# Optimization experiments

Hardware: AMD Instinct MI355X
Metric: run time of the kernel (lower is better)

The kernel has to match this reference:

```python
import jax, jax.numpy as jnp
import numpy as np

N, E, F_IN, NCLS, H = 50000, 800000, 128, 10, 64


def setup_inputs() -> dict:
    key = jax.random.key(0)
    ks = jax.random.split(key, 24)
    p = lambda k, shp: (jax.random.normal(k, shp, dtype=jnp.float32) * 0.1)
    inp = {
        'x': jax.random.normal(ks[0], (N, F_IN), dtype=jnp.float32),
        'edge_index': jax.random.randint(ks[1], (2, E), 0, N, dtype=jnp.int64),
        'gcn1_W': p(ks[2], (F_IN, 128)), 'gcn1_b': p(ks[3], (128,)),
        'gcn2_W': p(ks[4], (128, 64)),  'gcn2_b': p(ks[5], (64,)),
        'gcn3_W': p(ks[6], (64, 32)),   'gcn3_b': p(ks[7], (32,)),
        'gat_W': p(ks[8], (32, 32)), 'gat_a_src': p(ks[9], (32,)),
        'gat_a_dst': p(ks[10], (32,)), 'gat_b': p(ks[11], (32,)),
        'lstm_Wih_f': p(ks[12], (4 * H, 32)), 'lstm_bih_f': p(ks[13], (4 * H,)), 'lstm_bhh_f': p(ks[14], (4 * H,)),
        'lstm_Wih_b': p(ks[15], (4 * H, 32)), 'lstm_bih_b': p(ks[16], (4 * H,)), 'lstm_bhh_b': p(ks[17], (4 * H,)),
        'bn_gamma': jnp.ones((2 * H,), jnp.float32), 'bn_beta': jnp.zeros((2 * H,), jnp.float32),
        'fc_W': p(ks[18], (NCLS, 2 * H)), 'fc_b': p(ks[19], (NCLS,)),
    }
    return inp


def _forward(x, edge_index, gcn1_W, gcn1_b, gcn2_W, gcn2_b, gcn3_W, gcn3_b,
             gat_W, gat_a_src, gat_a_dst, gat_b,
             lstm_Wih_f, lstm_bih_f, lstm_bhh_f, lstm_Wih_b, lstm_bih_b, lstm_bhh_b,
             bn_gamma, bn_beta, fc_W, fc_b):
    n = x.shape[0]
    loop = jnp.arange(n)
    row = jnp.concatenate([edge_index[0], loop])  # source nodes (+ self loops)
    col = jnp.concatenate([edge_index[1], loop])  # target nodes
    deg = jax.ops.segment_sum(jnp.ones_like(col, dtype=x.dtype), col, num_segments=n)
    dis = jax.lax.rsqrt(jnp.maximum(deg, 1e-12))  # deg >= 1 due to self loops
    norm = dis[row] * dis[col]

    def gcn(h, W, b):
        h = h @ W
        return jax.ops.segment_sum(h[row] * norm[:, None], col, num_segments=n) + b

    h = jax.nn.relu(gcn(x, gcn1_W, gcn1_b))
    h = jax.nn.relu(gcn(h, gcn2_W, gcn2_b))
    h = gcn(h, gcn3_W, gcn3_b)

    # GAT (1 head), self loops already in row/col, softmax over incoming edges per target
    g = h @ gat_W
    e = jax.nn.leaky_relu((g @ gat_a_src)[row] + (g @ gat_a_dst)[col], negative_slope=0.2)
    m = jax.ops.segment_max(e, col, num_segments=n)
    ee = jnp.exp(e - m[col])
    att = ee / jax.ops.segment_sum(ee, col, num_segments=n)[col]
    h = jax.ops.segment_sum(g[row] * att[:, None], col, num_segments=n) + gat_b
    h = jax.nn.relu(h)

    # bidirectional LSTM with seq_len=1, h0=c0=0 -> single cell step per direction
    def lstm_dir(xx, Wih, bih, bhh):
        gt = xx @ Wih.T + bih + bhh
        i, f, c, o = jnp.split(gt, 4, axis=-1)  # torch gate order i,f,g,o
        return jax.nn.sigmoid(o) * jnp.tanh(jax.nn.sigmoid(i) * jnp.tanh(c))

    r = jnp.concatenate([lstm_dir(h, lstm_Wih_f, lstm_bih_f, lstm_bhh_f),
                         lstm_dir(h, lstm_Wih_b, lstm_bih_b, lstm_bhh_b)], axis=-1)
    # eval mode: dropout = identity; BatchNorm1d with running_mean=0, running_var=1
    r = r * (bn_gamma / jnp.sqrt(jnp.float32(1.0 + 1e-5))) + bn_beta
    return r @ fc_W.T + fc_b


def reference(x, edge_index, gcn1_W, gcn1_b, gcn2_W, gcn2_b, gcn3_W, gcn3_b,
              gat_W, gat_a_src, gat_a_dst, gat_b,
              lstm_Wih_f, lstm_bih_f, lstm_bhh_f, lstm_Wih_b, lstm_bih_b, lstm_bhh_b,
              bn_gamma, bn_beta, fc_W, fc_b):
    return _forward(x, edge_index, gcn1_W, gcn1_b, gcn2_W, gcn2_b, gcn3_W, gcn3_b,
                    gat_W, gat_a_src, gat_a_dst, gat_b,
                    lstm_Wih_f, lstm_bih_f, lstm_bhh_f, lstm_Wih_b, lstm_bih_b, lstm_bhh_b,
                    bn_gamma, bn_beta, fc_W, fc_b)
```

## Files before the change

### kernel.cpp

```cpp
#include <hip/hip_runtime.h>
#include <hip/hip_bf16.h>
#include <math.h>

typedef __hip_bfloat16 bf16;

#define NN 50000
#define EE 800000
#define EPB 4096
#define NBK 196
#define BCAP 6144

__device__ __forceinline__ float b2f(bf16 v) { return __bfloat162float(v); }
__device__ __forceinline__ float rcp_(float x) { return __builtin_amdgcn_rcpf(x); }
__device__ __forceinline__ float sigmoidf_(float x) { return rcp_(1.0f + __expf(-x)); }
__device__ __forceinline__ float tanhf_(float x) {
    float xx = fminf(fmaxf(x, -15.0f), 15.0f);
    float e = __expf(2.0f * xx);
    return (e - 1.0f) * rcp_(e + 1.0f);
}
__device__ __forceinline__ float leakyf_(float x) { return x > 0.0f ? x : 0.2f * x; }
__device__ __forceinline__ unsigned short f2bf(float f) {
    unsigned u = __float_as_uint(f);
    unsigned r = (u + 0x7FFFu + ((u >> 16) & 1u)) >> 16;
    return (unsigned short)r;
}
__device__ __forceinline__ unsigned pack2(float a, float b) {
    return (unsigned)f2bf(a) | ((unsigned)f2bf(b) << 16);
}
__device__ __forceinline__ float lo_(unsigned u) { return __uint_as_float(u << 16); }
__device__ __forceinline__ float hi_(unsigned u) { return __uint_as_float(u & 0xFFFF0000u); }

#define OFF_W1 0
#define OFF_B1 16384
#define OFF_W2 16512
#define OFF_B2 24704
#define OFF_W3 24768
#define OFF_B3 26816
#define OFF_GATW 26848
#define OFF_GAS 27872
#define OFF_GAD 27904
#define OFF_GAB 27936
#define OFF_WIHF 27968
#define OFF_BIHF 36160
#define OFF_BHHF 36416
#define OFF_WIHB 36672
#define OFF_BIHB 44864
#define OFF_BHHB 45120
#define OFF_GAMMA 45376
#define OFF_BETA 45504
#define OFF_FCW 45632
#define OFF_FCB 46912
#define WTOTAL 46922

struct WSrc { const void* p[20]; };

__global__ void k_detect(const unsigned short* __restrict__ xraw,
                         const unsigned int* __restrict__ eraw, int* __restrict__ flags) {
    __shared__ int f32f, i64f;
    int t = threadIdx.x;
    if (t == 0) { f32f = 0; i64f = 1; }
    __syncthreads();
    for (int i = t; i < 4096; i += 256) {
        unsigned short u = xraw[i];
        int ex = (u >> 7) & 0xFF;
        if (ex >= 0xC0) atomicOr(&f32f, 1);
        if (eraw[2 * i + 1] != 0u) atomicAnd(&i64f, 0);
    }
    __syncthreads();
    if (t == 0) { flags[0] = f32f; flags[1] = i64f; }
}

__global__ void k_cvt_w(WSrc srcs, float* __restrict__ dst, const int* __restrict__ flags,
                        int total) {
    constexpr int WOFF[21] = {OFF_W1,   OFF_B1,   OFF_W2,   OFF_B2,   OFF_W3,   OFF_B3,
                              OFF_GATW, OFF_GAS,  OFF_GAD,  OFF_GAB,  OFF_WIHF, OFF_BIHF,
                              OFF_BHHF, OFF_WIHB, OFF_BIHB, OFF_BHHB, OFF_GAMMA, OFF_BETA,
                              OFF_FCW,  OFF_FCB,  WTOTAL};
    int i = blockIdx.x * 256 + threadIdx.x;
    if (i >= total) return;
    int tn = 0;
#pragma unroll
    for (int j = 1; j < 20; ++j)
        if (i >= WOFF[j]) tn = j;
    int local = i - WOFF[tn];
    if (flags[0]) dst[i] = ((const float*)srcs.p[tn])[local];
    else dst[i] = b2f(((const bf16*)srcs.p[tn])[local]);
}

__global__ __launch_bounds__(256) void k_hist(const void* __restrict__ eraw,
                                              unsigned* __restrict__ gh,
                                              const int* __restrict__ flags) {
    __shared__ int h[256];
    int t = threadIdx.x, b = blockIdx.x;
    h[t] = 0;
    __syncthreads();
    int e0 = b * EPB;
    bool i64 = flags[1] != 0;
    for (int i = t; i < EPB; i += 256) {
        int e = e0 + i;
        if (e < EE) {
            int d = i64 ? (int)((const long long*)eraw)[EE + e] : ((const int*)eraw)[EE + e];
            d = min(max(d, 0), NN - 1);
            atomicAdd(&h[d >> 8], 1);
        }
    }
    __syncthreads();
    gh[b * 256 + t] = (unsigned)h[t];
}

__global__ __launch_bounds__(256) void k_bscan(const unsigned* __restrict__ gh,
                                               unsigned* __restrict__ gh2,
                                               int* __restrict__ bb, int* __restrict__ rptr) {
    __shared__ int s[256];
    int t = threadIdx.x;
    unsigned run = 0;
    for (int blk = 0; blk < NBK; ++blk) {
        unsigned v = gh[blk * 256 + t];
        gh2[blk * 256 + t] = run;
        run += v;
    }
    s[t] = (int)run;
    __syncthreads();
    for (int o = 1; o < 256; o <<= 1) {
        int x = (t >= o) ? s[t - o] : 0;
        __syncthreads();
        s[t] += x;
        __syncthreads();
    }
    bb[t] = s[t] - (int)run;
    if (t == 0) rptr[NN] = EE;
}

__global__ __launch_bounds__(256) void k_scatter(const void* __restrict__ eraw,
                                                 const unsigned* __restrict__ gh2,
                                                 const int* __restrict__ bb,
                                                 int2* __restrict__ ebkt,
                                                 const int* __restrict__ flags) {
    __shared__ unsigned cur[256];
    int t = threadIdx.x, b = blockIdx.x;
    cur[t] = gh2[b * 256 + t] + (unsigned)bb[t];
    __syncthreads();
    int e0 = b * EPB;
    bool i64 = flags[1] != 0;
    for (int i = t; i < EPB; i += 256) {
        int e = e0 + i;
        if (e < EE) {
            int sn, d;
            if (i64) {
                sn = (int)((const long long*)eraw)[e];
                d = (int)((const long long*)eraw)[EE + e];
            } else {
                sn = ((const int*)eraw)[e];
                d = ((const int*)eraw)[EE + e];
            }
            sn = min(max(sn, 0), NN - 1);
            d = min(max(d, 0), NN - 1);
            unsigned pos = atomicAdd(&cur[d >> 8], 1u);
            if (pos < (unsigned)EE) ebkt[pos] = make_int2(sn, d);
        }
    }
}

__global__ __launch_bounds__(256) void k_bucket_csr(const int2* __restrict__ ebkt,
                                                    const int* __restrict__ bb,
                                                    int* __restrict__ rptr,
                                                    float* __restrict__ dis,
                                                    int* __restrict__ csr_src) {
    __shared__ int hist[256];
    __shared__ int excl[256];
    __shared__ int cur[256];
    __shared__ int sorted[BCAP];
    int t = threadIdx.x, b = blockIdx.x;
    int s0 = bb[b], s1 = bb[b + 1];
    int len = min(s1 - s0, BCAP);
    hist[t] = 0;
    __syncthreads();
    for (int i = t; i < len; i += 256) atomicAdd(&hist[ebkt[s0 + i].y & 255], 1);
    __syncthreads();
    int v = hist[t];
    excl[t] = v;
    __syncthreads();
    for (int o = 1; o < 256; o <<= 1) {
        int x = (t >= o) ? excl[t - o] : 0;
        __syncthreads();
        excl[t] += x;
        __syncthreads();
    }
    int loc = excl[t] - v;
    int node = b * 256 + t;
    if (node < NN) {
        rptr[node] = s0 + loc;
        dis[node] = rsqrtf((float)(v + 1));
    }
    cur[t] = loc;
    __syncthreads();
    for (int i = t; i < len; i += 256) {
        int2 p = ebkt[s0 + i];
        int pos = atomicAdd(&cur[p.y & 255], 1);
        if (pos < BCAP) sorted[pos] = p.x;
    }
    __syncthreads();
    for (int i = t; i < len; i += 256) csr_src[s0 + i] = sorted[i];
}

template <int KIN, int KOUT, int MODE, bool SCALE>
__global__ __launch_bounds__(256) void k_tile_mm(const void* __restrict__ A,
                                                 const float* __restrict__ W,
                                                 unsigned* __restrict__ C, int n,
                                                 const int* __restrict__ flags, int want,
                                                 const float* __restrict__ dis) {
    if (want >= 0 && flags[0] != want) return;
    constexpr int BK = 32;
    constexpr int AST = BK + 4;
    constexpr int CPT = KOUT / 16;
    __shared__ float As[64 * AST];
    __shared__ float Ws[BK * KOUT];
    int t = threadIdx.x;
    int jc = t & 15;
    int ng = t >> 4;
    int base = blockIdx.x * 64;
    float acc[4][CPT];
#pragma unroll
    for (int i = 0; i < 4; ++i)
#pragma unroll
        for (int c = 0; c < CPT; ++c) acc[i][c] = 0.f;
    int snode = t >> 2;
    int gnode = min(base + snode, n - 1);
    int koff = (t & 3) * 8;
    for (int k0 = 0; k0 < KIN; k0 += BK) {
        {
            const float4* src = (const float4*)(W + k0 * KOUT);
            float4* dst = (float4*)Ws;
#pragma unroll
            for (int p = 0; p < BK * KOUT / 1024; ++p) dst[t + p * 256] = src[t + p * 256];
        }
        if (MODE == 0) {
            const unsigned* xr = (const unsigned*)A + (size_t)gnode * (KIN / 2) + (k0 + koff) / 2;
            unsigned u0 = xr[0], u1 = xr[1], u2 = xr[2], u3 = xr[3];
            float* d = As + snode * AST + koff;
            d[0] = lo_(u0); d[1] = hi_(u0);
            d[2] = lo_(u1); d[3] = hi_(u1);
            d[4] = lo_(u2); d[5] = hi_(u2);
            d[6] = lo_(u3); d[7] = hi_(u3);
        } else {
            const float4* ar = (const float4*)((const float*)A + (size_t)gnode * KIN + k0 + koff);
            float4 v0 = ar[0], v1 = ar[1];
            float4* d = (float4*)(As + snode * AST + koff);
            d[0] = v0;
            d[1] = v1;
        }
        __syncthreads();
#pragma unroll 8
        for (int k = 0; k < BK; ++k) {
            float w[CPT];
            const float* wr = Ws + k * KOUT + jc * CPT;
            if constexpr (CPT >= 4) {
#pragma unroll
                for (int c = 0; c < CPT; c += 4) {
                    float4 wv = *(const float4*)(wr + c);
                    w[c] = wv.x; w[c + 1] = wv.y; w[c + 2] = wv.z; w[c + 3] = wv.w;
                }
            } else {
                float2 wv = *(const float2*)wr;
                w[0] = wv.x; w[1] = wv.y;
            }
            float a0 = As[(ng * 4 + 0) * AST + k];
            float a1 = As[(ng * 4 + 1) * AST + k];
            float a2 = As[(ng * 4 + 2) * AST + k];
            float a3 = As[(ng * 4 + 3) * AST + k];
#pragma unroll
            for (int c = 0; c < CPT; ++c) {
                acc[0][c] += a0 * w[c];
                acc[1][c] += a1 * w[c];
                acc[2][c] += a2 * w[c];
                acc[3][c] += a3 * w[c];
            }
        }
        __syncthreads();
    }
#pragma unroll
    for (int i = 0; i < 4; ++i) {
        int node = base + ng * 4 + i;
        if (node < n) {
            float sc = SCALE ? dis[node] : 1.0f;
            unsigned* cr = C + (size_t)node * (KOUT / 2) + jc * (CPT / 2);
#pragma unroll
            for (int c = 0; c < CPT; c += 2)
                cr[c / 2] = pack2(acc[i][c] * sc, acc[i][c + 1] * sc);
        }
    }
}

template <bool RELU>
__global__ void k_agg128(const unsigned* __restrict__ t, const int* __restrict__ rptr,
                         const int* __restrict__ csr_src, const float* __restrict__ dis,
                         const float* __restrict__ bias, float* __restrict__ out, int n) {
    int wave = (blockIdx.x * blockDim.x + threadIdx.x) >> 6;
    int lane = threadIdx.x & 63;
    if (wave >= n) return;
    int dst = wave;
    float dd = dis[dst];
    float ax, ay;
    {
        unsigned u = t[(size_t)dst * 64 + lane];
        ax = lo_(u);
        ay = hi_(u);
    }
    int s = __builtin_amdgcn_readfirstlane(max(0, min(rptr[dst], EE)));
    int e = __builtin_amdgcn_readfirstlane(max(s, min(rptr[dst + 1], EE)));
    int j = s;
    for (; j + 8 <= e; j += 8) {
        int i0 = csr_src[j], i1 = csr_src[j + 1], i2 = csr_src[j + 2], i3 = csr_src[j + 3];
        int i4 = csr_src[j + 4], i5 = csr_src[j + 5], i6 = csr_src[j + 6], i7 = csr_src[j + 7];
        unsigned u0 = t[(size_t)i0 * 64 + lane], u1 = t[(size_t)i1 * 64 + lane];
        unsigned u2 = t[(size_t)i2 * 64 + lane], u3 = t[(size_t)i3 * 64 + lane];
        unsigned u4 = t[(size_t)i4 * 64 + lane], u5 = t[(size_t)i5 * 64 + lane];
        unsigned u6 = t[(size_t)i6 * 64 + lane], u7 = t[(size_t)i7 * 64 + lane];
        ax += (lo_(u0) + lo_(u1)) + (lo_(u2) + lo_(u3)) + (lo_(u4) + lo_(u5)) + (lo_(u6) + lo_(u7));
        ay += (hi_(u0) + hi_(u1)) + (hi_(u2) + hi_(u3)) + (hi_(u4) + hi_(u5)) + (hi_(u6) + hi_(u7));
    }
    for (; j + 4 <= e; j += 4) {
        int i0 = csr_src[j], i1 = csr_src[j + 1], i2 = csr_src[j + 2], i3 = csr_src[j + 3];
        unsigned u0 = t[(size_t)i0 * 64 + lane], u1 = t[(size_t)i1 * 64 + lane];
        unsigned u2 = t[(size_t)i2 * 64 + lane], u3 = t[(size_t)i3 * 64 + lane];
        ax += (lo_(u0) + lo_(u1)) + (lo_(u2) + lo_(u3));
        ay += (hi_(u0) + hi_(u1)) + (hi_(u2) + hi_(u3));
    }
    for (; j < e; ++j) {
        unsigned u0 = t[(size_t)csr_src[j] * 64 + lane];
        ax += lo_(u0);
        ay += hi_(u0);
    }
    float2 bv = *(const float2*)(bias + 2 * lane);
    float vx = ax * dd + bv.x;
    float vy = ay * dd + bv.y;
    if (RELU) { vx = fmaxf(vx, 0.f); vy = fmaxf(vy, 0.f); }
    *(float2*)(out + (size_t)dst * 128 + 2 * lane) = make_float2(vx, vy);
}

template <bool RELU>
__global__ void k_agg64(const unsigned* __restrict__ t, const int* __restrict__ rptr,
                        const int* __restrict__ csr_src, const float* __restrict__ dis,
                        const float* __restrict__ bias, float* __restrict__ out, int n) {
    int wave = (blockIdx.x * blockDim.x + threadIdx.x) >> 6;
    int lane = threadIdx.x & 63;
    if (wave >= n) return;
    int dst = wave;
    int half = lane >> 5, l32 = lane & 31;
    float dd = dis[dst];
    float ax = 0.f, ay = 0.f;
    if (!half) {
        unsigned u = t[(size_t)dst * 32 + l32];
        ax = lo_(u);
        ay = hi_(u);
    }
    int s = max(0, min(rptr[dst], EE));
    int e = max(s, min(rptr[dst + 1], EE));
    int cnt = e - s;
    int pairs = cnt >> 1;
    int p = 0;
    for (; p + 4 <= pairs; p += 4) {
        int jb = s + 2 * p + half;
        int i0 = csr_src[jb], i1 = csr_src[jb + 2], i2 = csr_src[jb + 4], i3 = csr_src[jb + 6];
        unsigned u0 = t[(size_t)i0 * 32 + l32], u1 = t[(size_t)i1 * 32 + l32];
        unsigned u2 = t[(size_t)i2 * 32 + l32], u3 = t[(size_t)i3 * 32 + l32];
        ax += (lo_(u0) + lo_(u1)) + (lo_(u2) + lo_(u3));
        ay += (hi_(u0) + hi_(u1)) + (hi_(u2) + hi_(u3));
    }
    for (; p < pairs; ++p) {
        int i0 = csr_src[s + 2 * p + half];
        unsigned u0 = t[(size_t)i0 * 32 + l32];
        ax += lo_(u0);
        ay += hi_(u0);
    }
    if ((cnt & 1) && !half) {
        unsigned u0 = t[(size_t)csr_src[e - 1] * 32 + l32];
        ax += lo_(u0);
        ay += hi_(u0);
    }
    ax += __shfl_down(ax, 32);
    ay += __shfl_down(ay, 32);
    if (!half) {
        float2 bv = *(const float2*)(bias + 2 * l32);
        float vx = ax * dd + bv.x;
        float vy = ay * dd + bv.y;
        if (RELU) { vx = fmaxf(vx, 0.f); vy = fmaxf(vy, 0.f); }
        *(float2*)(out + (size_t)dst * 64 + 2 * l32) = make_float2(vx, vy);
    }
}

template <bool RELU>
__global__ void k_agg32(const unsigned* __restrict__ t, const int* __restrict__ rptr,
                        const int* __restrict__ csr_src, const float* __restrict__ dis,
                        const float* __restrict__ bias, float* __restrict__ out, int n) {
    int wave = (blockIdx.x * blockDim.x + threadIdx.x) >> 6;
    int lane = threadIdx.x & 63;
    if (wave >= n) return;
    int dst = wave;
    int q = lane >> 4, l16 = lane & 15;
    float dd = dis[dst];
    float ax = 0.f, ay = 0.f;
    if (q == 0) {
        unsigned u = t[(size_t)dst * 16 + l16];
        ax = lo_(u);
        ay = hi_(u);
    }
    int s = max(0, min(rptr[dst], EE));
    int e = max(s, min(rptr[dst + 1], EE));
    int cnt = e - s;
    int quads = cnt >> 2;
    int p = 0;
    for (; p + 4 <= quads; p += 4) {
        int jb = s + 4 * p + q;
        int i0 = csr_src[jb], i1 = csr_src[jb + 4], i2 = csr_src[jb + 8], i3 = csr_src[jb + 12];
        unsigned u0 = t[(size_t)i0 * 16 + l16], u1 = t[(size_t)i1 * 16 + l16];
        unsigned u2 = t[(size_t)i2 * 16 + l16], u3 = t[(size_t)i3 * 16 + l16];
        ax += (lo_(u0) + lo_(u1)) + (lo_(u2) + lo_(u3));
        ay += (hi_(u0) + hi_(u1)) + (hi_(u2) + hi_(u3));
    }
    for (; p < quads; ++p) {
        int i0 = csr_src[s + 4 * p + q];
        unsigned u0 = t[(size_t)i0 * 16 + l16];
        ax += lo_(u0);
        ay += hi_(u0);
    }
    int rem = cnt - 4 * quads;
    if (q < rem) {
        unsigned u0 = t[(size_t)csr_src[s + 4 * quads + q] * 16 + l16];
        ax += lo_(u0);
        ay += hi_(u0);
    }
    ax += __shfl_down(ax, 32);
    ay += __shfl_down(ay, 32);
    ax += __shfl_down(ax, 16);
    ay += __shfl_down(ay, 16);
    if (q == 0) {
        float2 bv = *(const float2*)(bias + 2 * l16);
        float vx = ax * dd + bv.x;
        float vy = ay * dd + bv.y;
        if (RELU) { vx = fmaxf(vx, 0.f); vy = fmaxf(vy, 0.f); }
        *(float2*)(out + (size_t)dst * 32 + 2 * l16) = make_float2(vx, vy);
    }
}

__global__ void k_gat_vec(const unsigned* __restrict__ g, const float* __restrict__ a_src,
                          const float* __restrict__ a_dst, float* __restrict__ asrc,
                          float* __restrict__ adst, int n) {
    int i = blockIdx.x * 256 + threadIdx.x;
    if (i >= n) return;
    float s = 0.0f, d = 0.0f;
    const unsigned* gr = g + (size_t)i * 16;
#pragma unroll
    for (int k = 0; k < 16; ++k) {
        unsigned u = gr[k];
        float v0 = lo_(u), v1 = hi_(u);
        s += v0 * a_src[2 * k] + v1 * a_src[2 * k + 1];
        d += v0 * a_dst[2 * k] + v1 * a_dst[2 * k + 1];
    }
    asrc[i] = s;
    adst[i] = d;
}

__global__ void k_gat_agg(const unsigned* __restrict__ g, const int* __restrict__ rptr,
                          const int* __restrict__ csr_src, const float* __restrict__ asrc,
                          const float* __restrict__ adst, const float* __restrict__ gat_b,
                          float* __restrict__ out, int n) {
    int wave = (blockIdx.x * blockDim.x + threadIdx.x) >> 6;
    int lane = threadIdx.x & 63;
    if (wave >= n) return;
    int dst = wave;
    int q = lane >> 4, l16 = lane & 15;
    float ad = adst[dst];
    int s = max(0, min(rptr[dst], EE));
    int e = max(s, min(rptr[dst + 1], EE));
    float ax = 0.f, ay = 0.f, denom = 0.f;
    if (q == 0) {
        float w0 = __expf(fminf(leakyf_(asrc[dst] + ad), 80.f));
        unsigned u = g[(size_t)dst * 16 + l16];
        ax = lo_(u) * w0;
        ay = hi_(u) * w0;
        denom = w0;
    }
    int cnt = e - s;
    int quads = cnt >> 2;
    int p = 0;
    for (; p + 4 <= quads; p += 4) {
        int jb = s + 4 * p + q;
        int i0 = csr_src[jb], i1 = csr_src[jb + 4], i2 = csr_src[jb + 8], i3 = csr_src[jb + 12];
        float a0 = asrc[i0], a1 = asrc[i1], a2 = asrc[i2], a3 = asrc[i3];
        unsigned u0 = g[(size_t)i0 * 16 + l16], u1 = g[(size_t)i1 * 16 + l16];
        unsigned u2 = g[(size_t)i2 * 16 + l16], u3 = g[(size_t)i3 * 16 + l16];
        float w0 = __expf(fminf(leakyf_(a0 + ad), 80.f));
        float w1 = __expf(fminf(leakyf_(a1 + ad), 80.f));
        float w2 = __expf(fminf(leakyf_(a2 + ad), 80.f));
        float w3 = __expf(fminf(leakyf_(a3 + ad), 80.f));
        denom += (w0 + w1) + (w2 + w3);
        ax += lo_(u0) * w0 + lo_(u1) * w1 + lo_(u2) * w2 + lo_(u3) * w3;
        ay += hi_(u0) * w0 + hi_(u1) * w1 + hi_(u2) * w2 + hi_(u3) * w3;
    }
    for (; p < quads; ++p) {
        int i0 = csr_src[s + 4 * p + q];
        float wgt = __expf(fminf(leakyf_(asrc[i0] + ad), 80.f));
        unsigned u0 = g[(size_t)i0 * 16 + l16];
        denom += wgt;
        ax += lo_(u0) * wgt;
        ay += hi_(u0) * wgt;
    }
    int rem = cnt - 4 * quads;
    if (q < rem) {
        int i0 = csr_src[s + 4 * quads + q];
        float wgt = __expf(fminf(leakyf_(asrc[i0] + ad), 80.f));
        unsigned u0 = g[(size_t)i0 * 16 + l16];
        denom += wgt;
        ax += lo_(u0) * wgt;
        ay += hi_(u0) * wgt;
    }
    ax += __shfl_down(ax, 32);
    ay += __shfl_down(ay, 32);
    denom += __shfl_down(denom, 32);
    ax += __shfl_down(ax, 16);
    ay += __shfl_down(ay, 16);
    denom += __shfl_down(denom, 16);
    if (q == 0) {
        float r = rcp_(denom);
        float vx = fmaxf(ax * r + gat_b[2 * l16], 0.f);
        float vy = fmaxf(ay * r + gat_b[2 * l16 + 1], 0.f);
        *(float2*)(out + (size_t)dst * 32 + 2 * l16) = make_float2(vx, vy);
    }
}

__global__ __launch_bounds__(128) void k_lstm_fc(const float* __restrict__ h,
                                                 const float* __restrict__ wp,
                                                 void* __restrict__ out,
                                                 const int* __restrict__ flags, int n) {
    __shared__ float hs[32 * 32];
    __shared__ float rs[32 * 129];
    __shared__ float fcw[1280];
    __shared__ float ps[32 * 40];
    int t = threadIdx.x;
    int base = blockIdx.x * 32;
    for (int idx = t; idx < 256; idx += 128) {
        int nd = idx >> 3, k4 = idx & 7;
        int node = min(base + nd, n - 1);
        ((float4*)hs)[idx] = ((const float4*)(h + (size_t)node * 32))[k4];
    }
    for (int i = t; i < 1280; i += 128) fcw[i] = wp[OFF_FCW + i];
    __syncthreads();
    {
        int dir = t >> 6, j = t & 63;
        const float* W = wp + (dir ? OFF_WIHB : OFF_WIHF);
        const float* bi = wp + (dir ? OFF_BIHB : OFF_BIHF);
        const float* bh = wp + (dir ? OFF_BHHB : OFF_BHHF);
        float wi[32], wc[32], wo[32];
#pragma unroll
        for (int k = 0; k < 32; ++k) {
            wi[k] = W[j * 32 + k];
            wc[k] = W[(128 + j) * 32 + k];
            wo[k] = W[(192 + j) * 32 + k];
        }
        float bI = bi[j] + bh[j];
        float bC = bi[128 + j] + bh[128 + j];
        float bO = bi[192 + j] + bh[192 + j];
        float gsc = wp[OFF_GAMMA + t] * rsqrtf(1.0f + 1e-5f);
        float gbe = wp[OFF_BETA + t];
#pragma unroll 2
        for (int nn = 0; nn < 32; ++nn) {
            const float* hv = hs + nn * 32;
            float ai = bI, ac = bC, ao = bO;
#pragma unroll
            for (int k = 0; k < 32; ++k) {
                float hk = hv[k];
                ai += hk * wi[k];
                ac += hk * wc[k];
                ao += hk * wo[k];
            }
            float v = sigmoidf_(ao) * tanhf_(sigmoidf_(ai) * tanhf_(ac));
            rs[nn * 129 + t] = v * gsc + gbe;
        }
    }
    __syncthreads();
    {
        int nd = t & 31, q = t >> 5;
        float p10[10];
#pragma unroll
        for (int c = 0; c < 10; ++c) p10[c] = 0.f;
#pragma unroll
        for (int k = 0; k < 32; ++k) {
            float rv = rs[nd * 129 + q * 32 + k];
#pragma unroll
            for (int c = 0; c < 10; ++c) p10[c] += rv * fcw[c * 128 + q * 32 + k];
        }
#pragma unroll
        for (int c = 0; c < 10; ++c) ps[nd * 40 + q * 10 + c] = p10[c];
    }
    __syncthreads();
    for (int idx = t; idx < 320; idx += 128) {
        int nd = idx / 10, c = idx % 10;
        int node = base + nd;
        if (node < n) {
            float v = wp[OFF_FCB + c] + ps[nd * 40 + c] + ps[nd * 40 + 10 + c] +
                      ps[nd * 40 + 20 + c] + ps[nd * 40 + 30 + c];
            if (flags[0]) ((float*)out)[(size_t)node * 10 + c] = v;
            else ((bf16*)out)[(size_t)node * 10 + c] = __float2bfloat16(v);
        }
    }
}

extern "C" void kernel_launch(void* const* d_in, const int* in_sizes, int n_in,
                              void* d_out, int out_size, void* d_ws, size_t ws_size,
                              hipStream_t stream) {
    const int N = NN;

    char* w = (char*)d_ws;
    auto alloc = [&](size_t bytes) {
        void* p = (void*)w;
        w += (bytes + 255) & ~(size_t)255;
        return p;
    };
    int* flags = (int*)alloc(256);
    float* wpool = (float*)alloc((size_t)WTOTAL * 4);
    float* dis = (float*)alloc((size_t)N * 4);
    int* rptr = (int*)alloc((size_t)(N + 1) * 4);
    int* csr_src = (int*)alloc((size_t)EE * 4);
    unsigned* gh = (unsigned*)alloc((size_t)NBK * 256 * 4);
    unsigned* gh2 = (unsigned*)alloc((size_t)NBK * 256 * 4);
    int* bb = (int*)alloc(1024);
    int2* ebkt = (int2*)alloc((size_t)EE * 8);
    float* asrc = (float*)alloc((size_t)N * 4);
    float* adst = (float*)alloc((size_t)N * 4);
    unsigned* bufT = (unsigned*)alloc((size_t)N * 64 * 4);
    float* bufH = (float*)alloc((size_t)N * 128 * 4);

    WSrc ws_srcs;
    for (int i = 0; i < 20; ++i) ws_srcs.p[i] = d_in[2 + i];

    const int NB = (N + 255) / 256;
    const int AGG = (N + 3) / 4;
    const int TMB = (N + 63) / 64;
    const int LFB = (N + 31) / 32;
    const int WB = (WTOTAL + 255) / 256;

    k_detect<<<1, 256, 0, stream>>>((const unsigned short*)d_in[0],
                                    (const unsigned int*)d_in[1], flags);
    k_cvt_w<<<WB, 256, 0, stream>>>(ws_srcs, wpool, flags, WTOTAL);
    k_hist<<<NBK, 256, 0, stream>>>(d_in[1], gh, flags);
    k_bscan<<<1, 256, 0, stream>>>(gh, gh2, bb, rptr);
    k_scatter<<<NBK, 256, 0, stream>>>(d_in[1], gh2, bb, ebkt, flags);
    k_bucket_csr<<<NBK, 256, 0, stream>>>(ebkt, bb, rptr, dis, csr_src);

    k_tile_mm<128, 128, 0, true><<<TMB, 256, 0, stream>>>(d_in[0], wpool + OFF_W1, bufT, N, flags, 0, dis);
    k_tile_mm<128, 128, 1, true><<<TMB, 256, 0, stream>>>(d_in[0], wpool + OFF_W1, bufT, N, flags, 1, dis);
    k_agg128<true><<<AGG, 256, 0, stream>>>(bufT, rptr, csr_src, dis, wpool + OFF_B1, bufH, N);
    k_tile_mm<128, 64, 1, true><<<TMB, 256, 0, stream>>>(bufH, wpool + OFF_W2, bufT, N, flags, -1, dis);
    k_agg64<true><<<AGG, 256, 0, stream>>>(bufT, rptr, csr_src, dis, wpool + OFF_B2, bufH, N);
    k_tile_mm<64, 32, 1, true><<<TMB, 256, 0, stream>>>(bufH, wpool + OFF_W3, bufT, N, flags, -1, dis);
    k_agg32<false><<<AGG, 256, 0, stream>>>(bufT, rptr, csr_src, dis, wpool + OFF_B3, bufH, N);
    k_tile_mm<32, 32, 1, false><<<TMB, 256, 0, stream>>>(bufH, wpool + OFF_GATW, bufT, N, flags, -1, dis);
    k_gat_vec<<<NB, 256, 0, stream>>>(bufT, wpool + OFF_GAS, wpool + OFF_GAD, asrc, adst, N);
    k_gat_agg<<<AGG, 256, 0, stream>>>(bufT, rptr, csr_src, asrc, adst, wpool + OFF_GAB, bufH, N);
    k_lstm_fc<<<LFB, 128, 0, stream>>>(bufH, wpool, d_out, flags, N);
}
```

Before: 380.1 us.

## Split LSTM+FC into register-tiled gate GEMM kernel and separate FC kernel

Replaces the fused LSTM/FC kernel with a preprocessing step that packs the i/c/o gate weights into an interleaved layout. A register-tiled gate kernel then stages the weights in shared memory and computes 4 nodes x 24 gate columns per thread. This targets the low-reuse per-thread dot products in the old 128-thread kernel, where each thread held 96 weights in registers. The cost is a 128-float-per-node intermediate written to global memory and read back by a new FC kernel, plus the extra workspace buffers.

```diff
diff --git a/kernel.cpp b/kernel.cpp
--- a/kernel.cpp
+++ b/kernel.cpp
@@ -87,6 +87,29 @@
     else dst[i] = b2f(((const bf16*)srcs.p[tn])[local]);
 }
 
+__global__ void k_prep(const float* __restrict__ wp, float* __restrict__ wg,
+                       float* __restrict__ bg) {
+    int i = blockIdx.x * 256 + threadIdx.x;
+    if (i < 384) {
+        int jc = i / 24, rr = i % 24, r = rr / 3, g = rr % 3;
+        int f = jc * 8 + r;
+        int dir = f >> 6, j = f & 63;
+        int grow = (g == 0) ? j : ((g == 1) ? 128 + j : 192 + j);
+        int obi = dir ? OFF_BIHB : OFF_BIHF;
+        int obh = dir ? OFF_BHHB : OFF_BHHF;
+        bg[i] = wp[obi + grow] + wp[obh + grow];
+    }
+    if (i < 12288) {
+        int k = i / 384, col = i % 384;
+        int jc = col / 24, rr = col % 24, r = rr / 3, g = rr % 3;
+        int f = jc * 8 + r;
+        int dir = f >> 6, j = f & 63;
+        int grow = (g == 0) ? j : ((g == 1) ? 128 + j : 192 + j);
+        int ow = dir ? OFF_WIHB : OFF_WIHF;
+        wg[i] = wp[ow + grow * 32 + k];
+    }
+}
+
 __global__ __launch_bounds__(256) void k_hist(const void* __restrict__ eraw,
                                               unsigned* __restrict__ gh,
                                               const int* __restrict__ flags) {
@@ -287,6 +310,127 @@
 #pragma unroll
             for (int c = 0; c < CPT; c += 2)
                 cr[c / 2] = pack2(acc[i][c] * sc, acc[i][c + 1] * sc);
+        }
+    }
+}
+
+__global__ __launch_bounds__(256, 2) void k_gates(const float* __restrict__ h,
+                                                  const float* __restrict__ wg,
+                                                  const float* __restrict__ bg,
+                                                  const float* __restrict__ wp,
+                                                  float* __restrict__ r, int n) {
+    __shared__ float Ws[32 * 384];
+    __shared__ float As[64 * 36];
+    int t = threadIdx.x;
+    int jc = t & 15, ng = t >> 4;
+    int base = blockIdx.x * 64;
+    {
+        const float4* src = (const float4*)wg;
+        float4* dst = (float4*)Ws;
+#pragma unroll
+        for (int p = 0; p < 12; ++p) dst[t + p * 256] = src[t + p * 256];
+    }
+    {
+        int snode = t >> 2;
+        int gnode = min(base + snode, n - 1);
+        int koff = (t & 3) * 8;
+        const float4* ar = (const float4*)(h + (size_t)gnode * 32 + koff);
+        float4 v0 = ar[0], v1 = ar[1];
+        float4* d = (float4*)(As + snode * 36 + koff);
+        d[0] = v0;
+        d[1] = v1;
+    }
+    float acc[4][24];
+#pragma unroll
+    for (int c = 0; c < 24; ++c) {
+        float b = bg[jc * 24 + c];
+        acc[0][c] = b; acc[1][c] = b; acc[2][c] = b; acc[3][c] = b;
+    }
+    float gsc[8], gbe[8];
+    const float bnscale = rsqrtf(1.0f + 1e-5f);
+#pragma unroll
+    for (int rc = 0; rc < 8; ++rc) {
+        gsc[rc] = wp[OFF_GAMMA + jc * 8 + rc] * bnscale;
+        gbe[rc] = wp[OFF_BETA + jc * 8 + rc];
+    }
+    __syncthreads();
+#pragma unroll 4
+    for (int k = 0; k < 32; ++k) {
+        float w[24];
+        const float* wr = Ws + k * 384 + jc * 24;
+#pragma unroll
+        for (int c = 0; c < 24; c += 4) {
+            float4 wv = *(const float4*)(wr + c);
+            w[c] = wv.x; w[c + 1] = wv.y; w[c + 2] = wv.z; w[c + 3] = wv.w;
+        }
+        float a0 = As[(ng * 4 + 0) * 36 + k];
+        float a1 = As[(ng * 4 + 1) * 36 + k];
+        float a2 = As[(ng * 4 + 2) * 36 + k];
+        float a3 = As[(ng * 4 + 3) * 36 + k];
+#pragma unroll
+        for (int c = 0; c < 24; ++c) {
+            acc[0][c] += a0 * w[c];
+            acc[1][c] += a1 * w[c];
+            acc[2][c] += a2 * w[c];
+            acc[3][c] += a3 * w[c];
+        }
+    }
+#pragma unroll
+    for (int i = 0; i < 4; ++i) {
+        int node = base + ng * 4 + i;
+        if (node >= n) continue;
+        float vals[8];
+#pragma unroll
+        for (int rc = 0; rc < 8; ++rc) {
+            float gi = acc[i][3 * rc], gc = acc[i][3 * rc + 1], go = acc[i][3 * rc + 2];
+            float v = sigmoidf_(go) * tanhf_(sigmoidf_(gi) * tanhf_(gc));
+            vals[rc] = v * gsc[rc] + gbe[rc];
+        }
+        float* rr = r + (size_t)node * 128 + jc * 8;
+        *(float4*)rr = make_float4(vals[0], vals[1], vals[2], vals[3]);
+        *(float4*)(rr + 4) = make_float4(vals[4], vals[5], vals[6], vals[7]);
+    }
+}
+
+__global__ __launch_bounds__(256) void k_fc(const float* __restrict__ r,
+                                            const float* __restrict__ wp,
+                                            void* __restrict__ out,
+                                            const int* __restrict__ flags, int n) {
+    __shared__ float rt[64 * 132];
+    __shared__ float fcw[1280];
+    __shared__ float ps[64 * 40];
+    int t = threadIdx.x;
+    for (int i = t; i < 1280; i += 256) fcw[i] = wp[OFF_FCW + i];
+    int base = blockIdx.x * 64;
+    for (int idx = t; idx < 64 * 128; idx += 256) {
+        int nd = idx >> 7, k = idx & 127;
+        int node = min(base + nd, n - 1);
+        rt[nd * 132 + k] = r[(size_t)node * 128 + k];
+    }
+    __syncthreads();
+    {
+        int nd = t >> 2, q = t & 3;
+        float p[10];
+#pragma unroll
+        for (int c = 0; c < 10; ++c) p[c] = 0.f;
+#pragma unroll
+        for (int k = 0; k < 32; ++k) {
+            float rv = rt[nd * 132 + q * 32 + k];
+#pragma unroll
+            for (int c = 0; c < 10; ++c) p[c] += rv * fcw[c * 128 + q * 32 + k];
+        }
+#pragma unroll
+        for (int c = 0; c < 10; ++c) ps[nd * 40 + q * 10 + c] = p[c];
+    }
+    __syncthreads();
+    for (int idx = t; idx < 640; idx += 256) {
+        int nd = idx / 10, c = idx % 10;
+        int node = base + nd;
+        if (node < n) {
+            float v = wp[OFF_FCB + c] + ps[nd * 40 + c] + ps[nd * 40 + 10 + c] +
+                      ps[nd * 40 + 20 + c] + ps[nd * 40 + 30 + c];
+            if (flags[0]) ((float*)out)[(size_t)node * 10 + c] = v;
+            else ((bf16*)out)[(size_t)node * 10 + c] = __float2bfloat16(v);
         }
     }
 }
@@ -529,83 +673,6 @@
     }
 }
 
-__global__ __launch_bounds__(128) void k_lstm_fc(const float* __restrict__ h,
-                                                 const float* __restrict__ wp,
-                                                 void* __restrict__ out,
-                                                 const int* __restrict__ flags, int n) {
-    __shared__ float hs[32 * 32];
-    __shared__ float rs[32 * 129];
-    __shared__ float fcw[1280];
-    __shared__ float ps[32 * 40];
-    int t = threadIdx.x;
-    int base = blockIdx.x * 32;
-    for (int idx = t; idx < 256; idx += 128) {
-        int nd = idx >> 3, k4 = idx & 7;
-        int node = min(base + nd, n - 1);
-        ((float4*)hs)[idx] = ((const float4*)(h + (size_t)node * 32))[k4];
-    }
-    for (int i = t; i < 1280; i += 128) fcw[i] = wp[OFF_FCW + i];
-    __syncthreads();
-    {
-        int dir = t >> 6, j = t & 63;
-        const float* W = wp + (dir ? OFF_WIHB : OFF_WIHF);
-        const float* bi = wp + (dir ? OFF_BIHB : OFF_BIHF);
-        const float* bh = wp + (dir ? OFF_BHHB : OFF_BHHF);
-        float wi[32], wc[32], wo[32];
-#pragma unroll
-        for (int k = 0; k < 32; ++k) {
-            wi[k] = W[j * 32 + k];
-            wc[k] = W[(128 + j) * 32 + k];
-            wo[k] = W[(192 + j) * 32 + k];
-        }
-        float bI = bi[j] + bh[j];
-        float bC = bi[128 + j] + bh[128 + j];
-        float bO = bi[192 + j] + bh[192 + j];
-        float gsc = wp[OFF_GAMMA + t] * rsqrtf(1.0f + 1e-5f);
-        float gbe = wp[OFF_BETA + t];
-#pragma unroll 2
-        for (int nn = 0; nn < 32; ++nn) {
-            const float* hv = hs + nn * 32;
-            float ai = bI, ac = bC, ao = bO;
-#pragma unroll
-            for (int k = 0; k < 32; ++k) {
-                float hk = hv[k];
-                ai += hk * wi[k];
-                ac += hk * wc[k];
-                ao += hk * wo[k];
-            }
-            float v = sigmoidf_(ao) * tanhf_(sigmoidf_(ai) * tanhf_(ac));
-            rs[nn * 129 + t] = v * gsc + gbe;
-        }
-    }
-    __syncthreads();
-    {
-        int nd = t & 31, q = t >> 5;
-        float p10[10];
-#pragma unroll
-        for (int c = 0; c < 10; ++c) p10[c] = 0.f;
-#pragma unroll
-        for (int k = 0; k < 32; ++k) {
-            float rv = rs[nd * 129 + q * 32 + k];
-#pragma unroll
-            for (int c = 0; c < 10; ++c) p10[c] += rv * fcw[c * 128 + q * 32 + k];
-        }
-#pragma unroll
-        for (int c = 0; c < 10; ++c) ps[nd * 40 + q * 10 + c] = p10[c];
-    }
-    __syncthreads();
-    for (int idx = t; idx < 320; idx += 128) {
-        int nd = idx / 10, c = idx % 10;
-        int node = base + nd;
-        if (node < n) {
-            float v = wp[OFF_FCB + c] + ps[nd * 40 + c] + ps[nd * 40 + 10 + c] +
-                      ps[nd * 40 + 20 + c] + ps[nd * 40 + 30 + c];
-            if (flags[0]) ((float*)out)[(size_t)node * 10 + c] = v;
-            else ((bf16*)out)[(size_t)node * 10 + c] = __float2bfloat16(v);
-        }
-    }
-}
-
 extern "C" void kernel_launch(void* const* d_in, const int* in_sizes, int n_in,
                               void* d_out, int out_size, void* d_ws, size_t ws_size,
                               hipStream_t stream) {
@@ -619,6 +686,8 @@
     };
     int* flags = (int*)alloc(256);
     float* wpool = (float*)alloc((size_t)WTOTAL * 4);
+    float* wg = (float*)alloc(12288 * 4);
+    float* bg = (float*)alloc(384 * 4);
     float* dis = (float*)alloc((size_t)N * 4);
     int* rptr = (int*)alloc((size_t)(N + 1) * 4);
     int* csr_src = (int*)alloc((size_t)EE * 4);
@@ -628,6 +697,7 @@
     int2* ebkt = (int2*)alloc((size_t)EE * 8);
     float* asrc = (float*)alloc((size_t)N * 4);
     float* adst = (float*)alloc((size_t)N * 4);
+    float* hbuf = (float*)alloc((size_t)N * 32 * 4);
     unsigned* bufT = (unsigned*)alloc((size_t)N * 64 * 4);
     float* bufH = (float*)alloc((size_t)N * 128 * 4);
 
@@ -637,12 +707,12 @@
     const int NB = (N + 255) / 256;
     const int AGG = (N + 3) / 4;
     const int TMB = (N + 63) / 64;
-    const int LFB = (N + 31) / 32;
     const int WB = (WTOTAL + 255) / 256;
 
     k_detect<<<1, 256, 0, stream>>>((const unsigned short*)d_in[0],
                                     (const unsigned int*)d_in[1], flags);
     k_cvt_w<<<WB, 256, 0, stream>>>(ws_srcs, wpool, flags, WTOTAL);
+    k_prep<<<48, 256, 0, stream>>>(wpool, wg, bg);
     k_hist<<<NBK, 256, 0, stream>>>(d_in[1], gh, flags);
     k_bscan<<<1, 256, 0, stream>>>(gh, gh2, bb, rptr);
     k_scatter<<<NBK, 256, 0, stream>>>(d_in[1], gh2, bb, ebkt, flags);
@@ -654,9 +724,10 @@
     k_tile_mm<128, 64, 1, true><<<TMB, 256, 0, stream>>>(bufH, wpool + OFF_W2, bufT, N, flags, -1, dis);
     k_agg64<true><<<AGG, 256, 0, stream>>>(bufT, rptr, csr_src, dis, wpool + OFF_B2, bufH, N);
     k_tile_mm<64, 32, 1, true><<<TMB, 256, 0, stream>>>(bufH, wpool + OFF_W3, bufT, N, flags, -1, dis);
-    k_agg32<false><<<AGG, 256, 0, stream>>>(bufT, rptr, csr_src, dis, wpool + OFF_B3, bufH, N);
-    k_tile_mm<32, 32, 1, false><<<TMB, 256, 0, stream>>>(bufH, wpool + OFF_GATW, bufT, N, flags, -1, dis);
+    k_agg32<false><<<AGG, 256, 0, stream>>>(bufT, rptr, csr_src, dis, wpool + OFF_B3, hbuf, N);
+    k_tile_mm<32, 32, 1, false><<<TMB, 256, 0, stream>>>(hbuf, wpool + OFF_GATW, bufT, N, flags, -1, dis);
     k_gat_vec<<<NB, 256, 0, stream>>>(bufT, wpool + OFF_GAS, wpool + OFF_GAD, asrc, adst, N);
-    k_gat_agg<<<AGG, 256, 0, stream>>>(bufT, rptr, csr_src, asrc, adst, wpool + OFF_GAB, bufH, N);
-    k_lstm_fc<<<LFB, 128, 0, stream>>>(bufH, wpool, d_out, flags, N);
-}
+    k_gat_agg<<<AGG, 256, 0, stream>>>(bufT, rptr, csr_src, asrc, adst, wpool + OFF_GAB, hbuf, N);
+    k_gates<<<TMB, 256, 0, stream>>>(hbuf, wg, bg, wpool, bufH, N);
+    k_fc<<<TMB, 256, 0, stream>>>(bufH, wpool, d_out, flags, N);
+}
```

Measured after the change: 388.3 us. 1.02x slower.
